# Kernel optimization log

Hardware: AMD Instinct MI355X
Metric: run time of the kernel (lower is better)

The kernel has to match this reference:

```python
import jax, jax.numpy as jnp
import numpy as np

B, T, OUT = 2048, 512, 23
K = OUT + 2           # tags + START + STOP
START, STOP = OUT, OUT + 1
NEG = -10000.0


def setup_inputs() -> dict:
    key = jax.random.key(0)
    k1, k2, k3, k4 = jax.random.split(key, 4)
    feats = jax.random.normal(k1, (B, T, K), dtype=jnp.float32)
    tags = jax.random.randint(k2, (B, T), 0, OUT)            # gold labels, never START/STOP
    lengths = jax.random.randint(k3, (B,), 1, T + 1)          # at least 1 token
    transitions = jax.random.normal(k4, (K, K), dtype=jnp.float32)
    # as in __init__: no transition into START, none out of STOP
    transitions = transitions.at[START, :].set(NEG).at[:, STOP].set(NEG)
    return {"feats": feats, "tags": tags, "lengths": lengths, "transitions": transitions}


def reference(feats, tags, lengths, transitions):
    # Batched CRF negative log-likelihood: mean_b (forward_alg - score_sentence),
    # faithful to _forward_alg / _score_sentence with per-sequence lengths.
    Bb, Tt, Kk = feats.shape
    mask = jnp.arange(Tt)[None, :] < lengths[:, None]          # [B, T] bool

    # ---- forward algorithm (log partition) ----
    init = jnp.full((Bb, Kk), NEG, dtype=feats.dtype).at[:, START].set(0.0)

    def step(alpha, xs):
        feat_t, m_t = xs                                       # [B, K], [B]
        # next[b, j] = logsumexp_i(alpha[b, i] + trans[j, i]) + feat_t[b, j]
        nxt = jax.nn.logsumexp(alpha[:, None, :] + transitions[None, :, :], axis=-1) + feat_t
        return jnp.where(m_t[:, None], nxt, alpha), None

    alpha, _ = jax.lax.scan(step, init, (jnp.swapaxes(feats, 0, 1), mask.T))
    fwd_score = jax.nn.logsumexp(alpha + transitions[STOP][None, :], axis=-1)  # [B]

    # ---- gold path score ----
    tags_ext = jnp.concatenate(
        [jnp.full((Bb, 1), START, dtype=tags.dtype), tags], axis=1)            # [B, T+1]
    trans_sc = transitions[tags_ext[:, 1:], tags_ext[:, :-1]]                  # [B, T]
    emit_sc = jnp.take_along_axis(feats, tags[..., None], axis=-1)[..., 0]     # [B, T]
    last_tag = jnp.take_along_axis(tags, (lengths - 1)[:, None], axis=1)[:, 0] # [B]
    gold_score = jnp.sum((trans_sc + emit_sc) * mask, axis=1) + transitions[STOP, last_tag]

    return jnp.mean(fwd_score - gold_score)
```

## Files before the change

kernel.cpp:

```cpp
#include <hip/hip_runtime.h>


#define BB 2048
#define TT 512
#define KK 25
#define START_S 23
#define STOP_S 24

#define LOG2E 1.4426950408889634f
#define LN2   0.6931471805599453f

static __device__ __forceinline__ float fexp2(float x) { return __builtin_amdgcn_exp2f(x); }
static __device__ __forceinline__ float flog2(float x) { return __builtin_amdgcn_logf(x); }

static __device__ __forceinline__ void crf_step(
    float& A, float& g, int& tag_prev,
    const float* Mrow, const float* tlds,
    float fcur, float ef, int tagt, bool act, bool inK, int sl)
{
    const int ai = __float_as_int(A);
    float br[KK];
#define BC(J) br[J] = __int_as_float(__builtin_amdgcn_ds_swizzle(ai, ((J) << 5)));
    BC(0)  BC(1)  BC(2)  BC(3)  BC(4)
    BC(5)  BC(6)  BC(7)  BC(8)  BC(9)
    BC(10) BC(11) BC(12) BC(13) BC(14)
    BC(15) BC(16) BC(17) BC(18) BC(19)
    BC(20) BC(21) BC(22) BC(23) BC(24)
#undef BC

    float a0 = 0.f, a1 = 0.f, a2 = 0.f, a3 = 0.f;
    #pragma unroll
    for (int j = 0; j < 24; j += 4) {
        a0 = fmaf(Mrow[j],     br[j],     a0);
        a1 = fmaf(Mrow[j + 1], br[j + 1], a1);
        a2 = fmaf(Mrow[j + 2], br[j + 2], a2);
        a3 = fmaf(Mrow[j + 3], br[j + 3], a3);
    }
    a0 = fmaf(Mrow[24], br[24], a0);

    const float nxt = ((a0 + a1) + (a2 + a3)) * ef;
    A = (act && inK) ? nxt : A;
    if (act && sl == tagt) g += fcur + tlds[tagt * KK + tag_prev];
    if (act) tag_prev = tagt;
}

__global__ __launch_bounds__(64, 1) void crf_loss_kernel(
    const float* __restrict__ feats,
    const int*   __restrict__ tags,
    const int*   __restrict__ lengths,
    const float* __restrict__ trans,
    float*       __restrict__ out)
{
    __shared__ float tlds[KK * KK];

    const int lane = threadIdx.x & 63;
    for (int i = threadIdx.x; i < KK * KK; i += 64) tlds[i] = trans[i];
    __syncthreads();

    const int pair = blockIdx.x;
    const int half = lane >> 5;
    const int sl   = lane & 31;
    const int b    = pair * 2 + half;

    const int len  = lengths[b];
    const int lmax = max(lengths[pair * 2], lengths[pair * 2 + 1]);

    const float* fb = feats + (size_t)b * TT * KK;
    const int*   tb = tags  + (size_t)b * TT;

    const bool inK = sl < KK;
    const int rowbase = (inK ? sl : 0) * KK;
    float Mrow[KK];
    #pragma unroll
    for (int j = 0; j < KK; ++j) Mrow[j] = fexp2(tlds[rowbase + j] * LOG2E);

    float A = (sl == START_S) ? 1.0f : 0.0f;
    int   c2 = 0;
    float g  = 0.0f;
    int   tag_prev = START_S;

    const int fidx = inK ? sl : 0;

    float a00 = fb[0 * KK + fidx], a01 = fb[1 * KK + fidx];
    float a02 = fb[2 * KK + fidx], a03 = fb[3 * KK + fidx];
    int4  t0  = *(const int4*)tb;
    float a10 = fb[4 * KK + fidx], a11 = fb[5 * KK + fidx];
    float a12 = fb[6 * KK + fidx], a13 = fb[7 * KK + fidx];
    int4  t1  = *(const int4*)(tb + 4);

    const int ngroups = (lmax + 3) >> 2;

    #define RESCALE()                                                        \
    {                                                                        \
        float m = A;                                                         \
        m = fmaxf(m, __shfl_xor(m, 16));                                     \
        m = fmaxf(m, __shfl_xor(m, 8));                                      \
        m = fmaxf(m, __shfl_xor(m, 4));                                      \
        m = fmaxf(m, __shfl_xor(m, 2));                                      \
        m = fmaxf(m, __shfl_xor(m, 1));                                      \
        const int e = (int)(__float_as_uint(m) >> 23) - 127;                 \
        A *= __uint_as_float((unsigned)(127 - e) << 23);                     \
        c2 += e;                                                             \
    }

    #define DO_GROUP(BASE, F0, F1, F2, F3, T4)                               \
    {                                                                        \
        const float e0 = fexp2(F0 * LOG2E);                                  \
        const float e1 = fexp2(F1 * LOG2E);                                  \
        const float e2 = fexp2(F2 * LOG2E);                                  \
        const float e3 = fexp2(F3 * LOG2E);                                  \
        crf_step(A, g, tag_prev, Mrow, tlds, F0, e0, T4.x, (BASE) + 0 < len, inK, sl); \
        crf_step(A, g, tag_prev, Mrow, tlds, F1, e1, T4.y, (BASE) + 1 < len, inK, sl); \
        crf_step(A, g, tag_prev, Mrow, tlds, F2, e2, T4.z, (BASE) + 2 < len, inK, sl); \
        crf_step(A, g, tag_prev, Mrow, tlds, F3, e3, T4.w, (BASE) + 3 < len, inK, sl); \
        RESCALE();                                                           \
    }

    for (int gi = 0; gi < ngroups; gi += 2) {
        const int p2 = min((gi + 2) * 4, TT - 4);
        const int p3 = min((gi + 3) * 4, TT - 4);
        const float b00 = fb[(p2 + 0) * KK + fidx];
        const float b01 = fb[(p2 + 1) * KK + fidx];
        const float b02 = fb[(p2 + 2) * KK + fidx];
        const float b03 = fb[(p2 + 3) * KK + fidx];
        const int4  u2  = *(const int4*)(tb + p2);
        const float b10 = fb[(p3 + 0) * KK + fidx];
        const float b11 = fb[(p3 + 1) * KK + fidx];
        const float b12 = fb[(p3 + 2) * KK + fidx];
        const float b13 = fb[(p3 + 3) * KK + fidx];
        const int4  u3  = *(const int4*)(tb + p3);

        DO_GROUP(gi * 4,     a00, a01, a02, a03, t0);
        DO_GROUP(gi * 4 + 4, a10, a11, a12, a13, t1);

        a00 = b00; a01 = b01; a02 = b02; a03 = b03; t0 = u2;
        a10 = b10; a11 = b11; a12 = b12; a13 = b13; t1 = u3;
    }

    #undef DO_GROUP
    #undef RESCALE

    const float es = inK ? fexp2(tlds[STOP_S * KK + sl] * LOG2E) : 0.f;
    float w = (inK ? A : 0.f) * es;
    w += __shfl_xor(w, 16);
    w += __shfl_xor(w, 8);
    w += __shfl_xor(w, 4);
    w += __shfl_xor(w, 2);
    w += __shfl_xor(w, 1);
    const float fwd = (flog2(w) + (float)c2) * LN2;

    g += __shfl_xor(g, 16);
    g += __shfl_xor(g, 8);
    g += __shfl_xor(g, 4);
    g += __shfl_xor(g, 2);
    g += __shfl_xor(g, 1);

    if (sl == 0) {
        const float gold = g + tlds[STOP_S * KK + tag_prev];
        atomicAdd(out, (fwd - gold) * (1.0f / BB));
    }
}

extern "C" void kernel_launch(void* const* d_in, const int* in_sizes, int n_in,
                              void* d_out, int out_size, void* d_ws, size_t ws_size,
                              hipStream_t stream) {
    const float* feats   = (const float*)d_in[0];
    const int*   tags    = (const int*)d_in[1];
    const int*   lengths = (const int*)d_in[2];
    const float* trans   = (const float*)d_in[3];
    float* out = (float*)d_out;

    (void)hipMemsetAsync(out, 0, sizeof(float), stream);
    crf_loss_kernel<<<BB / 2, 64, 0, stream>>>(feats, tags, lengths, trans, out);
}
```

Baseline: 267.7 us.

## Use one wave per sequence with readlane broadcast and per-sequence length loop

Switches from packing two sequences into one 64-lane wave (32 lanes each, broadcast via ds_swizzle) to one sequence per wave, broadcasting alpha into scalar registers with readlane. The loop now runs exactly len steps per sequence with a remainder tail instead of masking to the pair's max length. Rescaling is folded into the next step's emission factor rather than done with a shuffle reduction. Doubles the number of blocks and leaves half of each wave's lanes idle, while removing per-step masking, cross-lane shuffles and wasted steps on the shorter sequence of each pair.

```diff
diff --git a/kernel.cpp b/kernel.cpp
--- a/kernel.cpp
+++ b/kernel.cpp
@@ -13,38 +13,7 @@
 static __device__ __forceinline__ float fexp2(float x) { return __builtin_amdgcn_exp2f(x); }
 static __device__ __forceinline__ float flog2(float x) { return __builtin_amdgcn_logf(x); }
 
-static __device__ __forceinline__ void crf_step(
-    float& A, float& g, int& tag_prev,
-    const float* Mrow, const float* tlds,
-    float fcur, float ef, int tagt, bool act, bool inK, int sl)
-{
-    const int ai = __float_as_int(A);
-    float br[KK];
-#define BC(J) br[J] = __int_as_float(__builtin_amdgcn_ds_swizzle(ai, ((J) << 5)));
-    BC(0)  BC(1)  BC(2)  BC(3)  BC(4)
-    BC(5)  BC(6)  BC(7)  BC(8)  BC(9)
-    BC(10) BC(11) BC(12) BC(13) BC(14)
-    BC(15) BC(16) BC(17) BC(18) BC(19)
-    BC(20) BC(21) BC(22) BC(23) BC(24)
-#undef BC
-
-    float a0 = 0.f, a1 = 0.f, a2 = 0.f, a3 = 0.f;
-    #pragma unroll
-    for (int j = 0; j < 24; j += 4) {
-        a0 = fmaf(Mrow[j],     br[j],     a0);
-        a1 = fmaf(Mrow[j + 1], br[j + 1], a1);
-        a2 = fmaf(Mrow[j + 2], br[j + 2], a2);
-        a3 = fmaf(Mrow[j + 3], br[j + 3], a3);
-    }
-    a0 = fmaf(Mrow[24], br[24], a0);
-
-    const float nxt = ((a0 + a1) + (a2 + a3)) * ef;
-    A = (act && inK) ? nxt : A;
-    if (act && sl == tagt) g += fcur + tlds[tagt * KK + tag_prev];
-    if (act) tag_prev = tagt;
-}
-
-__global__ __launch_bounds__(64, 1) void crf_loss_kernel(
+__global__ __launch_bounds__(64) void crf_loss_kernel(
     const float* __restrict__ feats,
     const int*   __restrict__ tags,
     const int*   __restrict__ lengths,
@@ -53,33 +22,77 @@
 {
     __shared__ float tlds[KK * KK];
 
-    const int lane = threadIdx.x & 63;
-    for (int i = threadIdx.x; i < KK * KK; i += 64) tlds[i] = trans[i];
+    const int lane = threadIdx.x;
+    for (int i = lane; i < KK * KK; i += 64) tlds[i] = trans[i];
     __syncthreads();
 
-    const int pair = blockIdx.x;
-    const int half = lane >> 5;
-    const int sl   = lane & 31;
-    const int b    = pair * 2 + half;
-
-    const int len  = lengths[b];
-    const int lmax = max(lengths[pair * 2], lengths[pair * 2 + 1]);
+    const int b   = blockIdx.x;
+    const int len = lengths[b];
 
     const float* fb = feats + (size_t)b * TT * KK;
     const int*   tb = tags  + (size_t)b * TT;
 
-    const bool inK = sl < KK;
-    const int rowbase = (inK ? sl : 0) * KK;
+    const bool inK  = lane < KK;
+    const int  fidx = inK ? lane : 0;
+
+    const int rowbase = fidx * KK;
     float Mrow[KK];
     #pragma unroll
     for (int j = 0; j < KK; ++j) Mrow[j] = fexp2(tlds[rowbase + j] * LOG2E);
 
-    float A = (sl == START_S) ? 1.0f : 0.0f;
+    float al[KK];
+    #pragma unroll
+    for (int j = 0; j < KK; ++j) al[j] = (j == START_S) ? 1.0f : 0.0f;
+
+    float A = 0.0f;
+    float scale = 1.0f;
     int   c2 = 0;
     float g  = 0.0f;
     int   tag_prev = START_S;
 
-    const int fidx = inK ? sl : 0;
+#define RL(J) al[J] = __int_as_float(__builtin_amdgcn_readlane(__float_as_int(A), J));
+#define RL_ALL() \
+    RL(0)  RL(1)  RL(2)  RL(3)  RL(4)  \
+    RL(5)  RL(6)  RL(7)  RL(8)  RL(9)  \
+    RL(10) RL(11) RL(12) RL(13) RL(14) \
+    RL(15) RL(16) RL(17) RL(18) RL(19) \
+    RL(20) RL(21) RL(22) RL(23) RL(24)
+
+#define STEP(F, EF, TAGT)                                                    \
+    {                                                                        \
+        float a0 = 0.f, a1 = 0.f, a2 = 0.f, a3 = 0.f;                        \
+        _Pragma("unroll")                                                    \
+        for (int j = 0; j < 24; j += 4) {                                    \
+            a0 = fmaf(Mrow[j],     al[j],     a0);                           \
+            a1 = fmaf(Mrow[j + 1], al[j + 1], a1);                           \
+            a2 = fmaf(Mrow[j + 2], al[j + 2], a2);                           \
+            a3 = fmaf(Mrow[j + 3], al[j + 3], a3);                           \
+        }                                                                    \
+        a0 = fmaf(Mrow[24], al[24], a0);                                     \
+        A = ((a0 + a1) + (a2 + a3)) * (EF);                                  \
+        RL_ALL();                                                            \
+        if (lane == (TAGT)) g += (F) + tlds[(TAGT) * KK + tag_prev];         \
+        tag_prev = (TAGT);                                                   \
+    }
+
+#define DO_GROUP(F0, F1, F2, F3, T4)                                         \
+    {                                                                        \
+        const float e0 = fexp2((F0) * LOG2E) * scale;                        \
+        const float e1 = fexp2((F1) * LOG2E);                                \
+        const float e2 = fexp2((F2) * LOG2E);                                \
+        const float e3 = fexp2((F3) * LOG2E);                                \
+        STEP(F0, e0, T4.x)                                                   \
+        STEP(F1, e1, T4.y)                                                   \
+        STEP(F2, e2, T4.z)                                                   \
+        STEP(F3, e3, T4.w)                                                   \
+        unsigned mx = 0u;                                                    \
+        _Pragma("unroll")                                                    \
+        for (int j = 0; j < KK; ++j)                                         \
+            mx = max(mx, (unsigned)__float_as_int(al[j]));                   \
+        const int e = (int)(mx >> 23) - 127;                                 \
+        scale = __uint_as_float((unsigned)(127 - e) << 23);                  \
+        c2 += e;                                                             \
+    }
 
     float a00 = fb[0 * KK + fidx], a01 = fb[1 * KK + fidx];
     float a02 = fb[2 * KK + fidx], a03 = fb[3 * KK + fidx];
@@ -88,37 +101,12 @@
     float a12 = fb[6 * KK + fidx], a13 = fb[7 * KK + fidx];
     int4  t1  = *(const int4*)(tb + 4);
 
-    const int ngroups = (lmax + 3) >> 2;
+    const int ngroups = len >> 2;
+    const int npairs  = ngroups >> 1;
 
-    #define RESCALE()                                                        \
-    {                                                                        \
-        float m = A;                                                         \
-        m = fmaxf(m, __shfl_xor(m, 16));                                     \
-        m = fmaxf(m, __shfl_xor(m, 8));                                      \
-        m = fmaxf(m, __shfl_xor(m, 4));                                      \
-        m = fmaxf(m, __shfl_xor(m, 2));                                      \
-        m = fmaxf(m, __shfl_xor(m, 1));                                      \
-        const int e = (int)(__float_as_uint(m) >> 23) - 127;                 \
-        A *= __uint_as_float((unsigned)(127 - e) << 23);                     \
-        c2 += e;                                                             \
-    }
-
-    #define DO_GROUP(BASE, F0, F1, F2, F3, T4)                               \
-    {                                                                        \
-        const float e0 = fexp2(F0 * LOG2E);                                  \
-        const float e1 = fexp2(F1 * LOG2E);                                  \
-        const float e2 = fexp2(F2 * LOG2E);                                  \
-        const float e3 = fexp2(F3 * LOG2E);                                  \
-        crf_step(A, g, tag_prev, Mrow, tlds, F0, e0, T4.x, (BASE) + 0 < len, inK, sl); \
-        crf_step(A, g, tag_prev, Mrow, tlds, F1, e1, T4.y, (BASE) + 1 < len, inK, sl); \
-        crf_step(A, g, tag_prev, Mrow, tlds, F2, e2, T4.z, (BASE) + 2 < len, inK, sl); \
-        crf_step(A, g, tag_prev, Mrow, tlds, F3, e3, T4.w, (BASE) + 3 < len, inK, sl); \
-        RESCALE();                                                           \
-    }
-
-    for (int gi = 0; gi < ngroups; gi += 2) {
-        const int p2 = min((gi + 2) * 4, TT - 4);
-        const int p3 = min((gi + 3) * 4, TT - 4);
+    for (int p = 0; p < npairs; ++p) {
+        const int p2 = min((p * 2 + 2) * 4, TT - 4);
+        const int p3 = min((p * 2 + 3) * 4, TT - 4);
         const float b00 = fb[(p2 + 0) * KK + fidx];
         const float b01 = fb[(p2 + 1) * KK + fidx];
         const float b02 = fb[(p2 + 2) * KK + fidx];
@@ -130,32 +118,49 @@
         const float b13 = fb[(p3 + 3) * KK + fidx];
         const int4  u3  = *(const int4*)(tb + p3);
 
-        DO_GROUP(gi * 4,     a00, a01, a02, a03, t0);
-        DO_GROUP(gi * 4 + 4, a10, a11, a12, a13, t1);
+        DO_GROUP(a00, a01, a02, a03, t0);
+        DO_GROUP(a10, a11, a12, a13, t1);
 
         a00 = b00; a01 = b01; a02 = b02; a03 = b03; t0 = u2;
         a10 = b10; a11 = b11; a12 = b12; a13 = b13; t1 = u3;
     }
+    if (ngroups & 1) {
+        DO_GROUP(a00, a01, a02, a03, t0);
+    }
 
-    #undef DO_GROUP
-    #undef RESCALE
+    const int base = len & ~3;
+    const int rem  = len & 3;
+    for (int k = 0; k < rem; ++k) {
+        const float f  = fb[(base + k) * KK + fidx];
+        const int   tg = tb[base + k];
+        const float ef = fexp2(f * LOG2E) * scale;
+        scale = 1.0f;
+        STEP(f, ef, tg)
+    }
 
-    const float es = inK ? fexp2(tlds[STOP_S * KK + sl] * LOG2E) : 0.f;
-    float w = (inK ? A : 0.f) * es;
+#undef DO_GROUP
+#undef STEP
+#undef RL_ALL
+#undef RL
+
+    const float es = inK ? fexp2(tlds[STOP_S * KK + lane] * LOG2E) : 0.f;
+    float w = inK ? (A * es) : 0.f;
+    w += __shfl_xor(w, 32);
     w += __shfl_xor(w, 16);
     w += __shfl_xor(w, 8);
     w += __shfl_xor(w, 4);
     w += __shfl_xor(w, 2);
     w += __shfl_xor(w, 1);
-    const float fwd = (flog2(w) + (float)c2) * LN2;
+    const float fwd = (flog2(w * scale) + (float)c2) * LN2;
 
+    g += __shfl_xor(g, 32);
     g += __shfl_xor(g, 16);
     g += __shfl_xor(g, 8);
     g += __shfl_xor(g, 4);
     g += __shfl_xor(g, 2);
     g += __shfl_xor(g, 1);
 
-    if (sl == 0) {
+    if (lane == 0) {
         const float gold = g + tlds[STOP_S * KK + tag_prev];
         atomicAdd(out, (fwd - gold) * (1.0f / BB));
     }
@@ -171,5 +176,5 @@
     float* out = (float*)d_out;
 
     (void)hipMemsetAsync(out, 0, sizeof(float), stream);
-    crf_loss_kernel<<<BB / 2, 64, 0, stream>>>(feats, tags, lengths, trans, out);
+    crf_loss_kernel<<<BB, 64, 0, stream>>>(feats, tags, lengths, trans, out);
 }
```

New measurement: 256.2 us. -4.3%, faster.
